# Kernel optimization log

Hardware: AMD Instinct MI355X
Metric: run time of the kernel (lower is better)

The kernel has to match this reference:

```python
import jax, jax.numpy as jnp
import numpy as np

B, NQ, NKV = 4, 2048, 2048
D_MODEL, N_HEADS, D_K = 1024, 16, 64


def setup_inputs() -> dict:
    key = jax.random.key(0)
    ks = jax.random.split(key, 7)
    s = 1.0 / np.sqrt(D_MODEL)
    return {
        "x": jax.random.normal(ks[0], (B, NQ, D_MODEL), jnp.float32),
        "encoding": jax.random.normal(ks[1], (B, NKV, D_MODEL), jnp.float32),
        "position_bias": jax.random.normal(ks[2], (1, N_HEADS, NQ, NKV), jnp.float32),
        "Wq": jax.random.normal(ks[3], (D_MODEL, D_MODEL), jnp.float32) * s,
        "Wk": jax.random.normal(ks[4], (D_MODEL, D_MODEL), jnp.float32) * s,
        "Wv": jax.random.normal(ks[5], (D_MODEL, D_MODEL), jnp.float32) * s,
        "Wo": jax.random.normal(ks[6], (D_MODEL, D_MODEL), jnp.float32) * s,
    }


def _split_heads(t):
    b, n, _ = t.shape
    return t.reshape(b, n, N_HEADS, D_K).transpose(0, 2, 1, 3)


def reference(x, encoding, position_bias, Wq, Wk, Wv, Wo):
    # Projections (flax Dense, no bias): y = x @ kernel
    Q = _split_heads(x @ Wq)            # [B,H,NQ,Dk]
    K = _split_heads(encoding @ Wk)     # [B,H,NKV,Dk]
    V = _split_heads(encoding @ Wv)     # [B,H,NKV,Dk]
    # T5-style: NO 1/sqrt(d_k) scaling; additive position bias before softmax
    scores = jnp.einsum('bhqd,bhkd->bhqk', Q, K) + position_bias
    attn = jax.nn.softmax(scores, axis=-1)
    ctx = jnp.einsum('bhqk,bhkd->bhqd', attn, V)    # [B,H,NQ,Dk]
    ctx = ctx.transpose(0, 2, 1, 3).reshape(x.shape[0], x.shape[1], D_MODEL)
    return ctx @ Wo
```

## Files before the change

kernel.cpp:

```cpp
#include <hip/hip_runtime.h>

#define B_   4
#define NQ_  2048
#define NKV_ 2048
#define H_   16
#define DK_  64
#define DM_  1024
#define DKV_ 2048

typedef _Float16 f16x8 __attribute__((ext_vector_type(8)));
typedef _Float16 f16x4 __attribute__((ext_vector_type(4)));
typedef float    f32x4 __attribute__((ext_vector_type(4)));

__device__ __forceinline__ void gload_lds16(const void* g, void* l) {
  __builtin_amdgcn_global_load_lds(
      (const __attribute__((address_space(1))) unsigned int*)g,
      (__attribute__((address_space(3))) unsigned int*)l, 16, 0, 0);
}

__global__ __launch_bounds__(256) void cast2_f16(const float* __restrict__ a,
                                                 const float* __restrict__ b,
                                                 _Float16* __restrict__ ao,
                                                 _Float16* __restrict__ bo) {
  int i = blockIdx.x * 256 + threadIdx.x;
  const float* in = (i < 2097152) ? a : b;
  _Float16* out = (i < 2097152) ? ao : bo;
  int j = i & 2097151;
  float4 v = ((const float4*)in)[j];
  f16x4 o = {(_Float16)v.x, (_Float16)v.y, (_Float16)v.z, (_Float16)v.w};
  *(f16x4*)(out + (size_t)j * 4) = o;
}

__global__ __launch_bounds__(256) void wtrans4(const float* __restrict__ Wq,
                                               const float* __restrict__ Wk,
                                               const float* __restrict__ Wv,
                                               const float* __restrict__ Wo,
                                               _Float16* __restrict__ WqT,
                                               _Float16* __restrict__ WkT,
                                               _Float16* __restrict__ WvT,
                                               _Float16* __restrict__ WoT) {
  __shared__ float tile[32][33];
  int which = blockIdx.x >> 10;
  const float* W = (which == 0) ? Wq : (which == 1) ? Wk : (which == 2) ? Wv : Wo;
  _Float16* Wt   = (which == 0) ? WqT : (which == 1) ? WkT : (which == 2) ? WvT : WoT;
  int idx = blockIdx.x & 1023;
  int bx = idx & 31, by = idx >> 5;
  int tx = threadIdx.x & 31, ty = threadIdx.x >> 5;
#pragma unroll
  for (int j = 0; j < 4; ++j)
    tile[ty + j * 8][tx] = W[(size_t)(by * 32 + ty + j * 8) * 1024 + bx * 32 + tx];
  __syncthreads();
#pragma unroll
  for (int j = 0; j < 4; ++j)
    Wt[(size_t)(bx * 32 + ty + j * 8) * 1024 + by * 32 + tx] = (_Float16)tile[tx][ty + j * 8];
}

template <int F32OUT>
__global__ __launch_bounds__(256, 2) void gemm_bt(const _Float16* __restrict__ A,
                                                  const _Float16* __restrict__ Bt,
                                                  void* __restrict__ Cp,
                                                  int M, int N, int K) {
  __shared__ _Float16 As[128 * 32];
  __shared__ _Float16 Bs[128 * 32];
  const int nbn = N >> 7;
  const int bm = blockIdx.x / nbn, bn = blockIdx.x % nbn;
  const int t = threadIdx.x, w = t >> 6, l = t & 63;
  const int lr = l & 15, lg = l >> 4;
  const int wr = w >> 1, wc = w & 1;
  const int m0 = bm << 7, n0 = bn << 7;

  f32x4 acc[4][4] = {};

  for (int k0 = 0; k0 < K; k0 += 32) {
#pragma unroll
    for (int p = 0; p < 2; ++p) {
      int off = p * 4096 + w * 1024 + l * 16;
      int row = off >> 6;
      int col = (off & 63) >> 1;
      gload_lds16(A  + (size_t)(m0 + row) * K + k0 + col, (char*)As + p * 4096 + w * 1024);
      gload_lds16(Bt + (size_t)(n0 + row) * K + k0 + col, (char*)Bs + p * 4096 + w * 1024);
    }
    __syncthreads();
    f16x8 af[4], bq[4];
#pragma unroll
    for (int i = 0; i < 4; ++i) {
      af[i] = *(const f16x8*)((const char*)As + (wr * 64 + i * 16 + lr) * 64 + lg * 16);
      bq[i] = *(const f16x8*)((const char*)Bs + (wc * 64 + i * 16 + lr) * 64 + lg * 16);
    }
#pragma unroll
    for (int i = 0; i < 4; ++i)
#pragma unroll
      for (int j = 0; j < 4; ++j)
        acc[i][j] = __builtin_amdgcn_mfma_f32_16x16x32_f16(af[i], bq[j], acc[i][j], 0, 0, 0);
    __syncthreads();
  }
#pragma unroll
  for (int i = 0; i < 4; ++i)
#pragma unroll
    for (int j = 0; j < 4; ++j)
#pragma unroll
      for (int r = 0; r < 4; ++r) {
        size_t row = m0 + wr * 64 + i * 16 + lg * 4 + r;
        size_t col = n0 + wc * 64 + j * 16 + lr;
        if (F32OUT) ((float*)Cp)[row * N + col] = acc[i][j][r];
        else ((_Float16*)Cp)[row * N + col] = (_Float16)acc[i][j][r];
      }
}

__global__ __launch_bounds__(256) void vtrans(const _Float16* __restrict__ KVb,
                                              _Float16* __restrict__ Vt) {
  __shared__ _Float16 tile[64][72];
  int idx = blockIdx.x;
  int kt = idx & 31, h = (idx >> 5) & 15, b = idx >> 9;
  int kv0 = kt << 6;
  int t = threadIdx.x;
#pragma unroll
  for (int p = 0; p < 2; ++p) {
    int c = t + p * 256;
    int row = c >> 3, cb = (c & 7) * 16;
    f16x8 v = *(const f16x8*)(KVb + (size_t)(b * NKV_ + kv0 + row) * DKV_ + 1024 + h * 64 + cb / 2);
    *(f16x8*)((char*)&tile[row][0] + cb) = v;
  }
  __syncthreads();
  int d = t & 63, j0 = (t >> 6) * 2;
#pragma unroll
  for (int jj = 0; jj < 2; ++jj) {
    int kvs = (j0 + jj) * 8;
    f16x8 o;
#pragma unroll
    for (int u = 0; u < 8; ++u) o[u] = tile[kvs + u][d];
    *(f16x8*)(Vt + ((size_t)((b * H_ + h) * 64 + d)) * NKV_ + kv0 + kvs) = o;
  }
}

__global__ __launch_bounds__(256, 4) void attn(const _Float16* __restrict__ Qb,
                                               const _Float16* __restrict__ KVb,
                                               const _Float16* __restrict__ Vt,
                                               const float* __restrict__ bias,
                                               _Float16* __restrict__ ctx) {
  __shared__ _Float16 Ks0[64 * 64];
  __shared__ _Float16 Ks1[64 * 64];
  __shared__ _Float16 Vs0[64 * 64];
  __shared__ _Float16 Vs1[64 * 64];
  __shared__ _Float16 Ps[4][16 * 64];
  const float LOG2E = 1.44269504f;
  int idx = blockIdx.x;
  int b = idx & 3, qt = (idx >> 2) & 31, hd = idx >> 7;
  int t = threadIdx.x, w = t >> 6, l = t & 63, lr = l & 15, lg = l >> 4;
  int qw = (qt << 6) + (w << 4);

  const _Float16* qp = Qb + (size_t)(b * NQ_ + qw + lr) * DM_ + hd * 64 + lg * 8;
  f16x8 aq0 = *(const f16x8*)qp;
  f16x8 aq1 = *(const f16x8*)(qp + 32);
#pragma unroll
  for (int u = 0; u < 8; ++u) { aq0[u] = aq0[u] * (_Float16)LOG2E; aq1[u] = aq1[u] * (_Float16)LOG2E; }

  f32x4 acc[4] = {};
  float mrow = -1e30f;
  float lsum = 0.f;

  const _Float16* Kbase = KVb + (size_t)b * NKV_ * DKV_ + hd * 64;
  const _Float16* Vtb   = Vt + (size_t)(b * H_ + hd) * 64 * NKV_;
  const float*    biasq = bias + ((size_t)hd * NQ_ + qw + lr) * NKV_ + lg * 4;

  const int srow = t >> 3;
  const int scb  = (t & 7) * 16;

  f16x8 kreg[2], vreg[2];

  auto LOADKV = [&](int kv0) {
#pragma unroll
    for (int p = 0; p < 2; ++p) {
      int row = srow + p * 32;
      kreg[p] = *(const f16x8*)(Kbase + (size_t)(kv0 + row) * DKV_ + scb / 2);
      vreg[p] = *(const f16x8*)(Vtb + (size_t)row * NKV_ + kv0 + scb / 2);
    }
  };
  auto WRITEKV = [&](_Float16* KsW, _Float16* VsW) {
#pragma unroll
    for (int p = 0; p < 2; ++p) {
      int row = srow + p * 32;
      int off = (row * 128 + scb) ^ ((row & 7) << 4);
      *(f16x8*)((char*)KsW + off) = kreg[p];
      *(f16x8*)((char*)VsW + off) = vreg[p];
    }
  };

  auto BODY = [&](const _Float16* KsR, const _Float16* VsR,
                  _Float16* KsW, _Float16* VsW, int it) {
    const int kv0 = it << 6;

    WRITEKV(KsW, VsW);

    int kvn = kv0 + 128;
    if (kvn > NKV_ - 64) kvn = NKV_ - 64;
    LOADKV(kvn);

    float4 bv4[4];
#pragma unroll
    for (int nt = 0; nt < 4; ++nt)
      bv4[nt] = *(const float4*)(biasq + kv0 + nt * 16);

    f32x4 s[4];
    __builtin_amdgcn_s_setprio(1);
#pragma unroll
    for (int nt = 0; nt < 4; ++nt) {
      int row = nt * 16 + lr;
      int sw = (row & 7) << 4;
      f16x8 kf0 = *(const f16x8*)((const char*)KsR + ((row * 128 + lg * 16) ^ sw));
      f16x8 kf1 = *(const f16x8*)((const char*)KsR + ((row * 128 + 64 + lg * 16) ^ sw));
      f32x4 z = {0.f, 0.f, 0.f, 0.f};
      z = __builtin_amdgcn_mfma_f32_16x16x32_f16(kf0, aq0, z, 0, 0, 0);
      s[nt] = __builtin_amdgcn_mfma_f32_16x16x32_f16(kf1, aq1, z, 0, 0, 0);
    }
    __builtin_amdgcn_s_setprio(0);

#pragma unroll
    for (int nt = 0; nt < 4; ++nt) {
      s[nt][0] = fmaf(bv4[nt].x, LOG2E, s[nt][0]);
      s[nt][1] = fmaf(bv4[nt].y, LOG2E, s[nt][1]);
      s[nt][2] = fmaf(bv4[nt].z, LOG2E, s[nt][2]);
      s[nt][3] = fmaf(bv4[nt].w, LOG2E, s[nt][3]);
    }

    float pmax = fmaxf(fmaxf(s[0][0], s[0][1]), fmaxf(s[0][2], s[0][3]));
#pragma unroll
    for (int nt = 1; nt < 4; ++nt)
      pmax = fmaxf(pmax, fmaxf(fmaxf(s[nt][0], s[nt][1]), fmaxf(s[nt][2], s[nt][3])));
    pmax = fmaxf(pmax, __shfl_xor(pmax, 16));
    pmax = fmaxf(pmax, __shfl_xor(pmax, 32));

    if (__any(pmax > mrow + 8.0f)) {
      float mn = fmaxf(mrow, pmax);
      float corr = exp2f(mrow - mn);
      mrow = mn;
      lsum *= corr;
#pragma unroll
      for (int nt = 0; nt < 4; ++nt)
#pragma unroll
        for (int r = 0; r < 4; ++r) acc[nt][r] *= corr;
    }

    float rs = 0.f;
#pragma unroll
    for (int nt = 0; nt < 4; ++nt)
#pragma unroll
      for (int r = 0; r < 4; ++r) {
        float p = exp2f(s[nt][r] - mrow);
        s[nt][r] = p;
        rs += p;
      }
    rs += __shfl_xor(rs, 16);
    rs += __shfl_xor(rs, 32);
    lsum += rs;

#pragma unroll
    for (int nt = 0; nt < 4; ++nt) {
      f16x4 pk = {(_Float16)s[nt][0], (_Float16)s[nt][1],
                  (_Float16)s[nt][2], (_Float16)s[nt][3]};
      int off = (lr * 128 + nt * 32 + lg * 8) ^ ((lr & 7) << 4);
      *(f16x4*)((char*)Ps[w] + off) = pk;
    }

    __builtin_amdgcn_s_setprio(1);
#pragma unroll
    for (int kk = 0; kk < 2; ++kk) {
      f16x8 pb = *(const f16x8*)((char*)Ps[w] +
                 ((lr * 128 + kk * 64 + lg * 16) ^ ((lr & 7) << 4)));
#pragma unroll
      for (int nt = 0; nt < 4; ++nt) {
        int row = nt * 16 + lr;
        f16x8 vf = *(const f16x8*)((const char*)VsR +
                 ((row * 128 + kk * 64 + lg * 16) ^ ((row & 7) << 4)));
        acc[nt] = __builtin_amdgcn_mfma_f32_16x16x32_f16(vf, pb, acc[nt], 0, 0, 0);
      }
    }
    __builtin_amdgcn_s_setprio(0);
    __syncthreads();
  };

  LOADKV(0);
  WRITEKV(Ks0, Vs0);
  LOADKV(64);
  __syncthreads();

  for (int i2 = 0; i2 < 16; ++i2) {
    BODY(Ks0, Vs0, Ks1, Vs1, i2 * 2);
    BODY(Ks1, Vs1, Ks0, Vs0, i2 * 2 + 1);
  }

  float inv = 1.0f / lsum;
#pragma unroll
  for (int nt = 0; nt < 4; ++nt) {
    f16x4 o = {(_Float16)(acc[nt][0] * inv), (_Float16)(acc[nt][1] * inv),
               (_Float16)(acc[nt][2] * inv), (_Float16)(acc[nt][3] * inv)};
    *(f16x4*)(ctx + ((size_t)b * NQ_ + qw + lr) * DM_ + hd * 64 + nt * 16 + lg * 4) = o;
  }
}

extern "C" void kernel_launch(void* const* d_in, const int* in_sizes, int n_in,
                              void* d_out, int out_size, void* d_ws, size_t ws_size,
                              hipStream_t stream) {
  const float* x    = (const float*)d_in[0];
  const float* enc  = (const float*)d_in[1];
  const float* bias = (const float*)d_in[2];
  const float* Wq   = (const float*)d_in[3];
  const float* Wk   = (const float*)d_in[4];
  const float* Wv   = (const float*)d_in[5];
  const float* Wo   = (const float*)d_in[6];
  char* ws = (char*)d_ws;
  const size_t MiB = 1024 * 1024;
  _Float16* WqT   = (_Float16*)(ws + 0 * MiB);
  _Float16* WkT   = (_Float16*)(ws + 2 * MiB);
  _Float16* WvT   = (_Float16*)(ws + 4 * MiB);
  _Float16* WoT   = (_Float16*)(ws + 6 * MiB);
  _Float16* xf    = (_Float16*)(ws + 8 * MiB);
  _Float16* encf  = (_Float16*)(ws + 24 * MiB);
  _Float16* Qb    = (_Float16*)(ws + 40 * MiB);
  _Float16* KVb   = (_Float16*)(ws + 56 * MiB);
  _Float16* Vt    = (_Float16*)(ws + 88 * MiB);
  _Float16* ctxf  = (_Float16*)(ws + 104 * MiB);

  wtrans4<<<4096, 256, 0, stream>>>(Wq, Wk, Wv, Wo, WqT, WkT, WvT, WoT);
  cast2_f16<<<16384, 256, 0, stream>>>(x, enc, xf, encf);
  gemm_bt<0><<<512, 256, 0, stream>>>(xf, WqT, Qb, 8192, 1024, 1024);
  gemm_bt<0><<<1024, 256, 0, stream>>>(encf, WkT, KVb, 8192, 2048, 1024);
  vtrans<<<2048, 256, 0, stream>>>(KVb, Vt);
  attn<<<2048, 256, 0, stream>>>(Qb, KVb, Vt, bias, ctxf);
  gemm_bt<1><<<512, 256, 0, stream>>>(ctxf, WoT, d_out, 8192, 1024, 1024);
}
```

Baseline: 350.5 us.

## Single-buffer K/V LDS with register prefetch and prefetch bias one tile ahead

Replaces the double-buffered K/V shared-memory tiles with a single buffer. Each iteration now writes its tile to LDS, syncs, then issues the register prefetch of the next tile. The position-bias loads are double-buffered in registers so the next tile's bias is requested while the current tile is being processed. The max reduction is rewritten as a shallower tree. This halves K/V LDS use, which may help occupancy, but adds a second barrier per iteration and shortens the prefetch distance from two tiles to one.

After: 345.7 us. About the same (-1.4%).

```diff
diff --git a/kernel.cpp b/kernel.cpp
--- a/kernel.cpp
+++ b/kernel.cpp
@@ -138,10 +138,8 @@
                                                const _Float16* __restrict__ Vt,
                                                const float* __restrict__ bias,
                                                _Float16* __restrict__ ctx) {
-  __shared__ _Float16 Ks0[64 * 64];
-  __shared__ _Float16 Ks1[64 * 64];
-  __shared__ _Float16 Vs0[64 * 64];
-  __shared__ _Float16 Vs1[64 * 64];
+  __shared__ _Float16 Ks[64 * 64];
+  __shared__ _Float16 Vs[64 * 64];
   __shared__ _Float16 Ps[4][16 * 64];
   const float LOG2E = 1.44269504f;
   int idx = blockIdx.x;
@@ -167,6 +165,7 @@
   const int scb  = (t & 7) * 16;
 
   f16x8 kreg[2], vreg[2];
+  float4 bvA[4], bvB[4];
 
   auto LOADKV = [&](int kv0) {
 #pragma unroll
@@ -176,30 +175,26 @@
       vreg[p] = *(const f16x8*)(Vtb + (size_t)row * NKV_ + kv0 + scb / 2);
     }
   };
-  auto WRITEKV = [&](_Float16* KsW, _Float16* VsW) {
+  auto LOADBIAS = [&](int kv0, float4 (&dst)[4]) {
+#pragma unroll
+    for (int nt = 0; nt < 4; ++nt)
+      dst[nt] = *(const float4*)(biasq + kv0 + nt * 16);
+  };
+
+  auto BODY = [&](float4 (&bv)[4], float4 (&bvn)[4], int it) {
+    const int kv0 = it << 6;
+
 #pragma unroll
     for (int p = 0; p < 2; ++p) {
       int row = srow + p * 32;
       int off = (row * 128 + scb) ^ ((row & 7) << 4);
-      *(f16x8*)((char*)KsW + off) = kreg[p];
-      *(f16x8*)((char*)VsW + off) = vreg[p];
-    }
-  };
-
-  auto BODY = [&](const _Float16* KsR, const _Float16* VsR,
-                  _Float16* KsW, _Float16* VsW, int it) {
-    const int kv0 = it << 6;
-
-    WRITEKV(KsW, VsW);
-
-    int kvn = kv0 + 128;
-    if (kvn > NKV_ - 64) kvn = NKV_ - 64;
+      *(f16x8*)((char*)Ks + off) = kreg[p];
+      *(f16x8*)((char*)Vs + off) = vreg[p];
+    }
+    __syncthreads();
+
+    const int kvn = (it < 31) ? kv0 + 64 : kv0;
     LOADKV(kvn);
-
-    float4 bv4[4];
-#pragma unroll
-    for (int nt = 0; nt < 4; ++nt)
-      bv4[nt] = *(const float4*)(biasq + kv0 + nt * 16);
 
     f32x4 s[4];
     __builtin_amdgcn_s_setprio(1);
@@ -207,8 +202,8 @@
     for (int nt = 0; nt < 4; ++nt) {
       int row = nt * 16 + lr;
       int sw = (row & 7) << 4;
-      f16x8 kf0 = *(const f16x8*)((const char*)KsR + ((row * 128 + lg * 16) ^ sw));
-      f16x8 kf1 = *(const f16x8*)((const char*)KsR + ((row * 128 + 64 + lg * 16) ^ sw));
+      f16x8 kf0 = *(const f16x8*)((char*)Ks + ((row * 128 + lg * 16) ^ sw));
+      f16x8 kf1 = *(const f16x8*)((char*)Ks + ((row * 128 + 64 + lg * 16) ^ sw));
       f32x4 z = {0.f, 0.f, 0.f, 0.f};
       z = __builtin_amdgcn_mfma_f32_16x16x32_f16(kf0, aq0, z, 0, 0, 0);
       s[nt] = __builtin_amdgcn_mfma_f32_16x16x32_f16(kf1, aq1, z, 0, 0, 0);
@@ -217,16 +212,21 @@
 
 #pragma unroll
     for (int nt = 0; nt < 4; ++nt) {
-      s[nt][0] = fmaf(bv4[nt].x, LOG2E, s[nt][0]);
-      s[nt][1] = fmaf(bv4[nt].y, LOG2E, s[nt][1]);
-      s[nt][2] = fmaf(bv4[nt].z, LOG2E, s[nt][2]);
-      s[nt][3] = fmaf(bv4[nt].w, LOG2E, s[nt][3]);
-    }
-
-    float pmax = fmaxf(fmaxf(s[0][0], s[0][1]), fmaxf(s[0][2], s[0][3]));
-#pragma unroll
-    for (int nt = 1; nt < 4; ++nt)
-      pmax = fmaxf(pmax, fmaxf(fmaxf(s[nt][0], s[nt][1]), fmaxf(s[nt][2], s[nt][3])));
+      s[nt][0] = fmaf(bv[nt].x, LOG2E, s[nt][0]);
+      s[nt][1] = fmaf(bv[nt].y, LOG2E, s[nt][1]);
+      s[nt][2] = fmaf(bv[nt].z, LOG2E, s[nt][2]);
+      s[nt][3] = fmaf(bv[nt].w, LOG2E, s[nt][3]);
+    }
+    LOADBIAS(kvn, bvn);
+
+    float m1 = fmaxf(fmaxf(s[0][0], s[0][1]), s[0][2]);
+    float m2 = fmaxf(fmaxf(s[0][3], s[1][0]), s[1][1]);
+    float m3 = fmaxf(fmaxf(s[1][2], s[1][3]), s[2][0]);
+    float m4 = fmaxf(fmaxf(s[2][1], s[2][2]), s[2][3]);
+    float m5 = fmaxf(fmaxf(s[3][0], s[3][1]), s[3][2]);
+    float m6 = fmaxf(fmaxf(m1, m2), s[3][3]);
+    float m7 = fmaxf(fmaxf(m3, m4), m5);
+    float pmax = fmaxf(m6, m7);
     pmax = fmaxf(pmax, __shfl_xor(pmax, 16));
     pmax = fmaxf(pmax, __shfl_xor(pmax, 32));
 
@@ -270,7 +270,7 @@
 #pragma unroll
       for (int nt = 0; nt < 4; ++nt) {
         int row = nt * 16 + lr;
-        f16x8 vf = *(const f16x8*)((const char*)VsR +
+        f16x8 vf = *(const f16x8*)((char*)Vs +
                  ((row * 128 + kk * 64 + lg * 16) ^ ((row & 7) << 4)));
         acc[nt] = __builtin_amdgcn_mfma_f32_16x16x32_f16(vf, pb, acc[nt], 0, 0, 0);
       }
@@ -280,13 +280,11 @@
   };
 
   LOADKV(0);
-  WRITEKV(Ks0, Vs0);
-  LOADKV(64);
-  __syncthreads();
+  LOADBIAS(0, bvA);
 
   for (int i2 = 0; i2 < 16; ++i2) {
-    BODY(Ks0, Vs0, Ks1, Vs1, i2 * 2);
-    BODY(Ks1, Vs1, Ks0, Vs0, i2 * 2 + 1);
+    BODY(bvA, bvB, i2 * 2);
+    BODY(bvB, bvA, i2 * 2 + 1);
   }
 
   float inv = 1.0f / lsum;
```
